# Kernel tuning notes

Hardware: AMD Instinct MI355X
Metric: run time of the kernel (lower is better)

Reference implementation:

```python
import jax, jax.numpy as jnp
import numpy as np

BN_EPS = 1e-5


def setup_inputs() -> dict:
    key = jax.random.key(0)
    k1, k2, k3 = jax.random.split(key, 3)
    N, C_IN, C_OUT, K = 200000, 32, 64, 27
    data_in = jax.random.normal(k1, (1, C_IN, N, 1), dtype=jnp.float32)
    # Octree neighbor table: for each octant, indices of its 27 (3x3x3) neighbors.
    # ocnn uses -1 for empty neighbors; indices here are all valid, but the
    # reference still masks negatives for faithfulness.
    neigh = jax.random.randint(k2, (N, K), 0, N, dtype=jnp.int64)
    weight = jax.random.normal(k3, (C_OUT, C_IN, K), dtype=jnp.float32) * 0.05
    bn_gamma = jnp.ones((C_OUT,), dtype=jnp.float32)
    bn_beta = jnp.zeros((C_OUT,), dtype=jnp.float32)
    return {"data_in": data_in, "neigh": neigh, "weight": weight,
            "bn_gamma": bn_gamma, "bn_beta": bn_beta}


def reference(data_in, neigh, weight, bn_gamma, bn_beta):
    # data_in: [1, C_in, N, 1] (ocnn octree feature layout)
    x = data_in[0, :, :, 0]                      # [C_in, N]
    valid = neigh >= 0                           # [N, 27]
    idx = jnp.where(valid, neigh, 0)
    # octree2col: gather 27 neighbor features per octant -> [C_in, N, 27]
    col = x[:, idx] * valid[None, :, :].astype(x.dtype)
    # grouped GEMM: weight [C_out, C_in, 27] contracted with col
    out = jnp.einsum('ock,cnk->on', weight, col)  # [C_out, N]
    # BatchNorm2d in training mode: batch stats over the node axis, biased var
    mean = jnp.mean(out, axis=1, keepdims=True)
    var = jnp.mean(jnp.square(out - mean), axis=1, keepdims=True)
    out = (out - mean) * jax.lax.rsqrt(var + BN_EPS)
    out = out * bn_gamma[:, None] + bn_beta[:, None]
    out = jax.nn.relu(out)
    return out[None, :, :, None]                 # [1, C_out, N, 1]
```

## Files before the change

kernel.cpp:

```cpp
#include <hip/hip_runtime.h>

#define N_PTS 200000
#define C_IN  32
#define C_OUT 64
#define K_NB  27
#define BN_EPS 1e-5f
#define CBLK  3125

using bf16x8 = __attribute__((ext_vector_type(8))) short;
using f32x4  = __attribute__((ext_vector_type(4))) float;

typedef const __attribute__((address_space(1))) char GP;
typedef __attribute__((address_space(3))) char LP;

#define M_WT_OFF  0
#define M_AB_OFF  114688
#define M_PS_OFF  131072
#define M_XT_OFF  2097152
#define M_WS_NEED ((size_t)M_XT_OFF + (size_t)(N_PTS + 1) * C_IN * 2)

#define F_WTK_OFF 0
#define F_AB_OFF  221184
#define F_PS_OFF  221824

__device__ __forceinline__ unsigned short f2bf(float f) {
    unsigned int u = __float_as_uint(f);
    u = (u + 0x7fffu + ((u >> 16) & 1u)) >> 16;
    return (unsigned short)u;
}

__global__ void k_prep(const float* __restrict__ x, const float* __restrict__ w,
                       unsigned short* __restrict__ xt, unsigned short* __restrict__ wt) {
    if (blockIdx.x < 782) {
        int n = blockIdx.x * 256 + threadIdx.x;
        if (n > N_PTS) return;
        unsigned short row[C_IN];
        if (n == N_PTS) {
#pragma unroll
            for (int c = 0; c < C_IN; ++c) row[c] = 0;
        } else {
#pragma unroll
            for (int c = 0; c < C_IN; ++c) row[c] = f2bf(x[(long long)c * N_PTS + n]);
        }
        uint4* dst = (uint4*)(xt + (long long)n * C_IN);
#pragma unroll
        for (int q = 0; q < 4; ++q) dst[q] = ((const uint4*)row)[q];
    } else {
        int i = (blockIdx.x - 782) * 256 + threadIdx.x;
        if (i >= 28 * C_OUT * C_IN) return;
        int c = i & 31, o = (i >> 5) & 63, k = i >> 11;
        wt[i] = (k < K_NB) ? f2bf(w[(o * C_IN + c) * K_NB + k]) : (unsigned short)0;
    }
}

__launch_bounds__(256, 5)
__global__ void k_conv_mfma(const unsigned short* __restrict__ xt,
                            const int* __restrict__ neigh,
                            const unsigned short* __restrict__ wt,
                            float* __restrict__ out,
                            float* __restrict__ ps) {
    __shared__ __align__(16) char lds_raw[6 * 4096 + K_NB * 64 * 4];
    char* bufB = lds_raw;
    int*  ntb  = (int*)(lds_raw + 24576);

    const int lane = threadIdx.x & 63;
    const int w    = threadIdx.x >> 6;
    const int l15  = lane & 15, lq = lane >> 4;
    const int n0   = blockIdx.x * 64;

    {
        int p  = threadIdx.x & 63;
        int kb = (threadIdx.x >> 6) * 7;
        const int* nrow = neigh + (long long)(n0 + p) * K_NB;
#pragma unroll
        for (int i = 0; i < 7; ++i) {
            int kk = kb + i;
            if (kk < K_NB) {
                int t = nrow[kk];
                ntb[kk * 64 + p] = ((unsigned)t < N_PTS) ? t : N_PTS;
            }
        }
    }
    __syncthreads();

    const char* xtb = (const char*)xt;
    const unsigned short* wtA = wt + w * 512 + l15 * 32 + lq * 8;
    const unsigned qoff = (unsigned)(lq * 16);

    unsigned bufB_a = (unsigned)(unsigned long long)(LP*)lds_raw;
    unsigned ntb_a  = bufB_a + 24576;
    unsigned badr   = bufB_a + (unsigned)(lq * 256 + l15 * 16);
    unsigned tadr   = ntb_a + (unsigned)(w * 64 + l15 * 4);

    f32x4 acc0 = {0.f,0.f,0.f,0.f}, acc1 = {0.f,0.f,0.f,0.f},
          acc2 = {0.f,0.f,0.f,0.f}, acc3 = {0.f,0.f,0.f,0.f};
    bf16x8 Ar[4];
    int tcur;

#define PSTEP(KK) \
    asm volatile("ds_read_b32 %0, %1 offset:%2" : "=v"(tcur) : "v"(tadr), "i"((KK)*256)); \
    asm volatile("s_waitcnt lgkmcnt(0)" ::: "memory"); \
    __builtin_amdgcn_sched_barrier(0); \
    __builtin_amdgcn_global_load_lds((GP*)(xtb + (unsigned long long)(unsigned)tcur * 64ull + qoff), \
        (LP*)(bufB + (KK)*4096 + w*1024), 16, 0, 0); \
    asm volatile("global_load_dwordx4 %0, %1, off" : "=v"(Ar[(KK)&3]) : "v"(wtA + (KK)*2048)); \
    __builtin_amdgcn_sched_barrier(0);

    PSTEP(0) PSTEP(1) PSTEP(2) PSTEP(3)
#undef PSTEP
    asm volatile("ds_read_b32 %0, %1 offset:%2" : "=v"(tcur) : "v"(tadr), "i"(4*256));

#define STEP(K, VM, PF, NT, LG) { \
    if (PF) { \
        asm volatile("s_waitcnt lgkmcnt(0)" ::: "memory"); \
        __builtin_amdgcn_sched_barrier(0); \
        __builtin_amdgcn_global_load_lds((GP*)(xtb + (unsigned long long)(unsigned)tcur * 64ull + qoff), \
            (LP*)(bufB + (((K)+4)%6)*4096 + w*1024), 16, 0, 0); \
    } \
    __builtin_amdgcn_sched_barrier(0); \
    asm volatile("s_waitcnt vmcnt(%0)" :: "i"(VM) : "memory"); \
    __builtin_amdgcn_sched_barrier(0); \
    asm volatile("s_barrier" ::: "memory"); \
    __builtin_amdgcn_sched_barrier(0); \
    bf16x8 b0, b1, b2, b3; \
    asm volatile("ds_read_b128 %0, %1 offset:%2" : "=v"(b0) : "v"(badr), "i"(((K)%6)*4096 + 0)); \
    asm volatile("ds_read_b128 %0, %1 offset:%2" : "=v"(b1) : "v"(badr), "i"(((K)%6)*4096 + 1024)); \
    asm volatile("ds_read_b128 %0, %1 offset:%2" : "=v"(b2) : "v"(badr), "i"(((K)%6)*4096 + 2048)); \
    asm volatile("ds_read_b128 %0, %1 offset:%2" : "=v"(b3) : "v"(badr), "i"(((K)%6)*4096 + 3072)); \
    if (NT) { asm volatile("ds_read_b32 %0, %1 offset:%2" : "=v"(tcur) : "v"(tadr), "i"(((K)+5)*256)); } \
    asm volatile("s_waitcnt lgkmcnt(%0)" :: "i"(LG) : "memory"); \
    __builtin_amdgcn_sched_barrier(0); \
    acc0 = __builtin_amdgcn_mfma_f32_16x16x32_bf16(Ar[(K)&3], b0, acc0, 0, 0, 0); \
    acc1 = __builtin_amdgcn_mfma_f32_16x16x32_bf16(Ar[(K)&3], b1, acc1, 0, 0, 0); \
    acc2 = __builtin_amdgcn_mfma_f32_16x16x32_bf16(Ar[(K)&3], b2, acc2, 0, 0, 0); \
    acc3 = __builtin_amdgcn_mfma_f32_16x16x32_bf16(Ar[(K)&3], b3, acc3, 0, 0, 0); \
    if (PF) { \
        asm volatile("global_load_dwordx4 %0, %1, off" : "=v"(Ar[((K)+4)&3]) : "v"(wtA + ((K)+4)*2048)); \
    } \
    __builtin_amdgcn_sched_barrier(0); \
}

    STEP(0,7,1,1,1)  STEP(1,7,1,1,1)  STEP(2,7,1,1,1)  STEP(3,7,1,1,1)
    STEP(4,7,1,1,1)  STEP(5,7,1,1,1)  STEP(6,7,1,1,1)  STEP(7,7,1,1,1)
    STEP(8,7,1,1,1)  STEP(9,7,1,1,1)  STEP(10,7,1,1,1) STEP(11,7,1,1,1)
    STEP(12,7,1,1,1) STEP(13,7,1,1,1) STEP(14,7,1,1,1) STEP(15,7,1,1,1)
    STEP(16,7,1,1,1) STEP(17,7,1,1,1) STEP(18,7,1,1,1) STEP(19,7,1,1,1)
    STEP(20,7,1,1,1) STEP(21,7,1,1,1) STEP(22,7,1,0,0)
    STEP(23,6,0,0,0) STEP(24,4,0,0,0) STEP(25,2,0,0,0) STEP(26,0,0,0,0)
#undef STEP

    asm volatile("s_waitcnt vmcnt(0) lgkmcnt(0)" ::: "memory");
    __builtin_amdgcn_sched_barrier(0);

#pragma unroll
    for (int r = 0; r < 4; ++r) {
        float* o = out + (long long)(16 * w + lq * 4 + r) * N_PTS + n0 + l15;
        o[0]  = acc0[r];
        o[16] = acc1[r];
        o[32] = acc2[r];
        o[48] = acc3[r];
    }

    f32x4 s  = acc0 + acc1 + acc2 + acc3;
    f32x4 sq = acc0 * acc0 + acc1 * acc1 + acc2 * acc2 + acc3 * acc3;
#pragma unroll
    for (int d = 1; d < 16; d <<= 1) {
#pragma unroll
        for (int r = 0; r < 4; ++r) {
            s[r]  += __shfl_xor(s[r], d);
            sq[r] += __shfl_xor(sq[r], d);
        }
    }
    if (l15 == 0) {
#pragma unroll
        for (int r = 0; r < 4; ++r) {
            int ch = 16 * w + lq * 4 + r;
            ps[blockIdx.x * 128 + ch]      = s[r];
            ps[blockIdx.x * 128 + 64 + ch] = sq[r];
        }
    }
}

__global__ void k_stats2(const float* __restrict__ ps, const float* __restrict__ gamma,
                         const float* __restrict__ beta, float* __restrict__ ab) {
    int ch = blockIdx.x;
    float s = 0.f, s2 = 0.f;
    for (int b = threadIdx.x; b < CBLK; b += 256) {
        s  += ps[b * 128 + ch];
        s2 += ps[b * 128 + 64 + ch];
    }
#pragma unroll
    for (int off = 32; off > 0; off >>= 1) {
        s  += __shfl_down(s, off, 64);
        s2 += __shfl_down(s2, off, 64);
    }
    __shared__ float r0[4], r1[4];
    int wv = threadIdx.x >> 6;
    if ((threadIdx.x & 63) == 0) { r0[wv] = s; r1[wv] = s2; }
    __syncthreads();
    if (threadIdx.x == 0) {
        float S  = r0[0] + r0[1] + r0[2] + r0[3];
        float S2 = r1[0] + r1[1] + r1[2] + r1[3];
        float mean = S / (float)N_PTS;
        float var  = S2 / (float)N_PTS - mean * mean;
        float a = gamma[ch] * rsqrtf(var + BN_EPS);
        float b = beta[ch] - mean * a;
        ab[ch]      = a;
        ab[64 + ch] = b;
    }
}

__global__ void k_norm(float* __restrict__ out, const float* __restrict__ ab) {
    int i = blockIdx.x * 256 + threadIdx.x;
    const int total4 = (C_OUT * N_PTS) / 4;
    if (i >= total4) return;
    int o = (i * 4) / N_PTS;
    float a = ab[o], b = ab[64 + o];
    float4 v = ((float4*)out)[i];
    v.x = fmaxf(fmaf(v.x, a, b), 0.f);
    v.y = fmaxf(fmaf(v.y, a, b), 0.f);
    v.z = fmaxf(fmaf(v.z, a, b), 0.f);
    v.w = fmaxf(fmaf(v.w, a, b), 0.f);
    ((float4*)out)[i] = v;
}

__global__ void k_wt_f32(const float* __restrict__ w, float* __restrict__ wtk) {
    int i = blockIdx.x * 256 + threadIdx.x;
    if (i >= K_NB * C_IN * C_OUT) return;
    int o = i & 63, r = i >> 6, c = r & 31, k = r >> 5;
    wtk[i] = w[(o * C_IN + c) * K_NB + k];
}

__launch_bounds__(256, 1)
__global__ void k_conv_f32(const float* __restrict__ src, const int* __restrict__ neigh,
                           const float* __restrict__ wtk, float* __restrict__ out) {
    __shared__ float wt_s[C_IN * C_OUT];
    const int lane = threadIdx.x & 63;
    const int wave = threadIdx.x >> 6;
    const int n0   = blockIdx.x * 64 + wave * 16;
    float acc[16];
#pragma unroll
    for (int p = 0; p < 16; ++p) acc[p] = 0.f;
    for (int k = 0; k < K_NB; ++k) {
        __syncthreads();
#pragma unroll
        for (int j = 0; j < 8; ++j)
            wt_s[threadIdx.x + j * 256] = wtk[k * (C_IN * C_OUT) + threadIdx.x + j * 256];
        __syncthreads();
        int t[16];
#pragma unroll
        for (int p = 0; p < 16; ++p) t[p] = neigh[(n0 + p) * K_NB + k];
#pragma unroll
        for (int c = 0; c < C_IN; ++c) {
            float wv = wt_s[c * C_OUT + lane];
#pragma unroll
            for (int p = 0; p < 16; ++p) {
                float xv = (t[p] >= 0) ? src[(long long)c * N_PTS + t[p]] : 0.f;
                acc[p] = fmaf(wv, xv, acc[p]);
            }
        }
    }
    float4* dst = (float4*)(out + (long long)lane * N_PTS + n0);
#pragma unroll
    for (int q = 0; q < 4; ++q) dst[q] = ((const float4*)acc)[q];
}

__global__ void k_stats1(const float* __restrict__ raw, float* __restrict__ ps) {
    int o = blockIdx.x & 63, sl = blockIdx.x >> 6;
    const int per = N_PTS / 8;
    const float4* row = (const float4*)(raw + (long long)o * N_PTS + (long long)sl * per);
    float s = 0.f, s2 = 0.f;
    for (int i = threadIdx.x; i < per / 4; i += 256) {
        float4 v = row[i];
        s  += v.x + v.y + v.z + v.w;
        s2 += v.x * v.x + v.y * v.y + v.z * v.z + v.w * v.w;
    }
#pragma unroll
    for (int off = 32; off > 0; off >>= 1) {
        s  += __shfl_down(s, off, 64);
        s2 += __shfl_down(s2, off, 64);
    }
    __shared__ float r0[4], r1[4];
    int wv = threadIdx.x >> 6;
    if ((threadIdx.x & 63) == 0) { r0[wv] = s; r1[wv] = s2; }
    __syncthreads();
    if (threadIdx.x == 0) {
        ps[blockIdx.x]       = r0[0] + r0[1] + r0[2] + r0[3];
        ps[512 + blockIdx.x] = r1[0] + r1[1] + r1[2] + r1[3];
    }
}

__global__ void k_stats2f(const float* __restrict__ ps, const float* __restrict__ gamma,
                          const float* __restrict__ beta, float* __restrict__ ab) {
    int o = threadIdx.x;
    float S = 0.f, S2 = 0.f;
#pragma unroll
    for (int sl = 0; sl < 8; ++sl) {
        S  += ps[sl * 64 + o];
        S2 += ps[512 + sl * 64 + o];
    }
    float mean = S / (float)N_PTS;
    float var  = S2 / (float)N_PTS - mean * mean;
    float a = gamma[o] * rsqrtf(var + BN_EPS);
    float b = beta[o] - mean * a;
    ab[o]      = a;
    ab[64 + o] = b;
}

extern "C" void kernel_launch(void* const* d_in, const int* in_sizes, int n_in,
                              void* d_out, int out_size, void* d_ws, size_t ws_size,
                              hipStream_t stream) {
    const float* x   = (const float*)d_in[0];
    const int*   nb  = (const int*)d_in[1];
    const float* w   = (const float*)d_in[2];
    const float* gam = (const float*)d_in[3];
    const float* bet = (const float*)d_in[4];
    float* out = (float*)d_out;
    char* ws = (char*)d_ws;

    if (ws_size >= M_WS_NEED) {
        unsigned short* wt = (unsigned short*)(ws + M_WT_OFF);
        float*          ab = (float*)(ws + M_AB_OFF);
        float*          ps = (float*)(ws + M_PS_OFF);
        unsigned short* xt = (unsigned short*)(ws + M_XT_OFF);

        k_prep<<<1006, 256, 0, stream>>>(x, w, xt, wt);
        k_conv_mfma<<<CBLK, 256, 0, stream>>>(xt, nb, wt, out, ps);
        k_stats2<<<C_OUT, 256, 0, stream>>>(ps, gam, bet, ab);
        k_norm<<<((C_OUT * N_PTS) / 4 + 255) / 256, 256, 0, stream>>>(out, ab);
    } else {
        float* wtk  = (float*)(ws + F_WTK_OFF);
        float* ab   = (float*)(ws + F_AB_OFF);
        float* ps   = (float*)(ws + F_PS_OFF);
        k_wt_f32<<<(K_NB * C_IN * C_OUT + 255) / 256, 256, 0, stream>>>(w, wtk);
        k_conv_f32<<<N_PTS / 64, 256, 0, stream>>>(x, nb, wtk, out);
        k_stats1<<<512, 256, 0, stream>>>(out, ps);
        k_stats2f<<<1, 64, 0, stream>>>(ps, gam, bet, ab);
        k_norm<<<((C_OUT * N_PTS) / 4 + 255) / 256, 256, 0, stream>>>(out, ab);
    }
}
```

Baseline: 127.7 us.

## Split bf16 features into four channel-quarter planes and regroup the gather by quarter

Stores the bf16 transposed features as four separate planes of 8 channels each (16 B per point) rather than one 64 B row per point. Each MFMA step now gathers one channel quarter for four different neighbour offsets, with the weights repacked to match and a padded 28th offset. The aim is to shrink the per-plane gather footprint so random neighbour reads hit cache better. In exchange the loop runs one extra step, the LDS index table grows, and each lane's 16 B access now falls in a separate 64 B region.

```diff
diff --git a/kernel.cpp b/kernel.cpp
--- a/kernel.cpp
+++ b/kernel.cpp
@@ -6,6 +6,7 @@
 #define K_NB  27
 #define BN_EPS 1e-5f
 #define CBLK  3125
+#define TBYTES 3200016ull
 
 using bf16x8 = __attribute__((ext_vector_type(8))) short;
 using f32x4  = __attribute__((ext_vector_type(4))) float;
@@ -17,7 +18,7 @@
 #define M_AB_OFF  114688
 #define M_PS_OFF  131072
 #define M_XT_OFF  2097152
-#define M_WS_NEED ((size_t)M_XT_OFF + (size_t)(N_PTS + 1) * C_IN * 2)
+#define M_WS_NEED ((size_t)M_XT_OFF + 4ull * TBYTES)
 
 #define F_WTK_OFF 0
 #define F_AB_OFF  221184
@@ -30,7 +31,7 @@
 }
 
 __global__ void k_prep(const float* __restrict__ x, const float* __restrict__ w,
-                       unsigned short* __restrict__ xt, unsigned short* __restrict__ wt) {
+                       unsigned short* __restrict__ xtq, unsigned short* __restrict__ wt2) {
     if (blockIdx.x < 782) {
         int n = blockIdx.x * 256 + threadIdx.x;
         if (n > N_PTS) return;
@@ -42,24 +43,32 @@
 #pragma unroll
             for (int c = 0; c < C_IN; ++c) row[c] = f2bf(x[(long long)c * N_PTS + n]);
         }
-        uint4* dst = (uint4*)(xt + (long long)n * C_IN);
-#pragma unroll
-        for (int q = 0; q < 4; ++q) dst[q] = ((const uint4*)row)[q];
+#pragma unroll
+        for (int cq = 0; cq < 4; ++cq) {
+            uint4* dst = (uint4*)((char*)xtq + (size_t)cq * TBYTES + (size_t)n * 16);
+            *dst = ((const uint4*)row)[cq];
+        }
     } else {
         int i = (blockIdx.x - 782) * 256 + threadIdx.x;
-        if (i >= 28 * C_OUT * C_IN) return;
-        int c = i & 31, o = (i >> 5) & 63, k = i >> 11;
-        wt[i] = (k < K_NB) ? f2bf(w[(o * C_IN + c) * K_NB + k]) : (unsigned short)0;
+        if (i >= 28 * 2048) return;
+        int j  = i & 7;
+        int lq = (i >> 3) & 3;
+        int o  = (i >> 5) & 63;
+        int s  = i >> 11;
+        int cq = s / 7, k4 = s % 7;
+        int kk = 4 * k4 + lq;
+        int c  = cq * 8 + j;
+        wt2[i] = (kk < K_NB) ? f2bf(w[(o * C_IN + c) * K_NB + kk]) : (unsigned short)0;
     }
 }
 
 __launch_bounds__(256, 5)
-__global__ void k_conv_mfma(const unsigned short* __restrict__ xt,
+__global__ void k_conv_mfma(const unsigned short* __restrict__ xtq,
                             const int* __restrict__ neigh,
-                            const unsigned short* __restrict__ wt,
+                            const unsigned short* __restrict__ wt2,
                             float* __restrict__ out,
                             float* __restrict__ ps) {
-    __shared__ __align__(16) char lds_raw[6 * 4096 + K_NB * 64 * 4];
+    __shared__ __align__(16) char lds_raw[6 * 4096 + 28 * 64 * 4];
     char* bufB = lds_raw;
     int*  ntb  = (int*)(lds_raw + 24576);
 
@@ -75,22 +84,19 @@
 #pragma unroll
         for (int i = 0; i < 7; ++i) {
             int kk = kb + i;
-            if (kk < K_NB) {
-                int t = nrow[kk];
-                ntb[kk * 64 + p] = ((unsigned)t < N_PTS) ? t : N_PTS;
-            }
+            int t  = (kk < K_NB) ? nrow[kk] : N_PTS;
+            ntb[kk * 64 + p] = ((unsigned)t < N_PTS) ? t : N_PTS;
         }
     }
     __syncthreads();
 
-    const char* xtb = (const char*)xt;
-    const unsigned short* wtA = wt + w * 512 + l15 * 32 + lq * 8;
-    const unsigned qoff = (unsigned)(lq * 16);
+    const char* xtb = (const char*)xtq;
+    const unsigned short* wtA = wt2 + w * 512 + l15 * 32 + lq * 8;
 
     unsigned bufB_a = (unsigned)(unsigned long long)(LP*)lds_raw;
     unsigned ntb_a  = bufB_a + 24576;
     unsigned badr   = bufB_a + (unsigned)(lq * 256 + l15 * 16);
-    unsigned tadr   = ntb_a + (unsigned)(w * 64 + l15 * 4);
+    unsigned tadr   = ntb_a + (unsigned)(lq * 256 + w * 64 + l15 * 4);
 
     f32x4 acc0 = {0.f,0.f,0.f,0.f}, acc1 = {0.f,0.f,0.f,0.f},
           acc2 = {0.f,0.f,0.f,0.f}, acc3 = {0.f,0.f,0.f,0.f};
@@ -98,23 +104,23 @@
     int tcur;
 
 #define PSTEP(KK) \
-    asm volatile("ds_read_b32 %0, %1 offset:%2" : "=v"(tcur) : "v"(tadr), "i"((KK)*256)); \
+    asm volatile("ds_read_b32 %0, %1 offset:%2" : "=v"(tcur) : "v"(tadr), "i"(((KK)%7)*1024)); \
     asm volatile("s_waitcnt lgkmcnt(0)" ::: "memory"); \
     __builtin_amdgcn_sched_barrier(0); \
-    __builtin_amdgcn_global_load_lds((GP*)(xtb + (unsigned long long)(unsigned)tcur * 64ull + qoff), \
+    __builtin_amdgcn_global_load_lds((GP*)(xtb + (size_t)(((KK)/7)) * TBYTES + (unsigned long long)(unsigned)tcur * 16ull), \
         (LP*)(bufB + (KK)*4096 + w*1024), 16, 0, 0); \
     asm volatile("global_load_dwordx4 %0, %1, off" : "=v"(Ar[(KK)&3]) : "v"(wtA + (KK)*2048)); \
     __builtin_amdgcn_sched_barrier(0);
 
     PSTEP(0) PSTEP(1) PSTEP(2) PSTEP(3)
 #undef PSTEP
-    asm volatile("ds_read_b32 %0, %1 offset:%2" : "=v"(tcur) : "v"(tadr), "i"(4*256));
+    asm volatile("ds_read_b32 %0, %1 offset:%2" : "=v"(tcur) : "v"(tadr), "i"((4%7)*1024));
 
 #define STEP(K, VM, PF, NT, LG) { \
     if (PF) { \
         asm volatile("s_waitcnt lgkmcnt(0)" ::: "memory"); \
         __builtin_amdgcn_sched_barrier(0); \
-        __builtin_amdgcn_global_load_lds((GP*)(xtb + (unsigned long long)(unsigned)tcur * 64ull + qoff), \
+        __builtin_amdgcn_global_load_lds((GP*)(xtb + (size_t)((((K)+4)/7)) * TBYTES + (unsigned long long)(unsigned)tcur * 16ull), \
             (LP*)(bufB + (((K)+4)%6)*4096 + w*1024), 16, 0, 0); \
     } \
     __builtin_amdgcn_sched_barrier(0); \
@@ -127,7 +133,7 @@
     asm volatile("ds_read_b128 %0, %1 offset:%2" : "=v"(b1) : "v"(badr), "i"(((K)%6)*4096 + 1024)); \
     asm volatile("ds_read_b128 %0, %1 offset:%2" : "=v"(b2) : "v"(badr), "i"(((K)%6)*4096 + 2048)); \
     asm volatile("ds_read_b128 %0, %1 offset:%2" : "=v"(b3) : "v"(badr), "i"(((K)%6)*4096 + 3072)); \
-    if (NT) { asm volatile("ds_read_b32 %0, %1 offset:%2" : "=v"(tcur) : "v"(tadr), "i"(((K)+5)*256)); } \
+    if (NT) { asm volatile("ds_read_b32 %0, %1 offset:%2" : "=v"(tcur) : "v"(tadr), "i"(((((K)+5)%7))*1024)); } \
     asm volatile("s_waitcnt lgkmcnt(%0)" :: "i"(LG) : "memory"); \
     __builtin_amdgcn_sched_barrier(0); \
     acc0 = __builtin_amdgcn_mfma_f32_16x16x32_bf16(Ar[(K)&3], b0, acc0, 0, 0, 0); \
@@ -145,8 +151,8 @@
     STEP(8,7,1,1,1)  STEP(9,7,1,1,1)  STEP(10,7,1,1,1) STEP(11,7,1,1,1)
     STEP(12,7,1,1,1) STEP(13,7,1,1,1) STEP(14,7,1,1,1) STEP(15,7,1,1,1)
     STEP(16,7,1,1,1) STEP(17,7,1,1,1) STEP(18,7,1,1,1) STEP(19,7,1,1,1)
-    STEP(20,7,1,1,1) STEP(21,7,1,1,1) STEP(22,7,1,0,0)
-    STEP(23,6,0,0,0) STEP(24,4,0,0,0) STEP(25,2,0,0,0) STEP(26,0,0,0,0)
+    STEP(20,7,1,1,1) STEP(21,7,1,1,1) STEP(22,7,1,1,1) STEP(23,7,1,0,0)
+    STEP(24,6,0,0,0) STEP(25,4,0,0,0) STEP(26,2,0,0,0) STEP(27,0,0,0,0)
 #undef STEP
 
     asm volatile("s_waitcnt vmcnt(0) lgkmcnt(0)" ::: "memory");
@@ -319,13 +325,13 @@
     char* ws = (char*)d_ws;
 
     if (ws_size >= M_WS_NEED) {
-        unsigned short* wt = (unsigned short*)(ws + M_WT_OFF);
-        float*          ab = (float*)(ws + M_AB_OFF);
-        float*          ps = (float*)(ws + M_PS_OFF);
-        unsigned short* xt = (unsigned short*)(ws + M_XT_OFF);
-
-        k_prep<<<1006, 256, 0, stream>>>(x, w, xt, wt);
-        k_conv_mfma<<<CBLK, 256, 0, stream>>>(xt, nb, wt, out, ps);
+        unsigned short* wt2 = (unsigned short*)(ws + M_WT_OFF);
+        float*          ab  = (float*)(ws + M_AB_OFF);
+        float*          ps  = (float*)(ws + M_PS_OFF);
+        unsigned short* xtq = (unsigned short*)(ws + M_XT_OFF);
+
+        k_prep<<<1006, 256, 0, stream>>>(x, w, xtq, wt2);
+        k_conv_mfma<<<CBLK, 256, 0, stream>>>(xtq, nb, wt2, out, ps);
         k_stats2<<<C_OUT, 256, 0, stream>>>(ps, gam, bet, ab);
         k_norm<<<((C_OUT * N_PTS) / 4 + 255) / 256, 256, 0, stream>>>(out, ab);
     } else {
```

Measured after the change: 230.6 us. 1.81x slower.
